# Kernel optimization log

Measured on AMD Instinct MI355X. Metric: run time of the kernel, lower is better.

Reference implementation:

```python
import jax, jax.numpy as jnp
import numpy as np

BINS = 8
EPS = 1e-12  # torch F.normalize default eps


def _pairwise_scores(matf):
    # torch: input1[a,b]=matf[b]; transpose(0,1)->matf[a]; transpose(-2,-1)->matf[a]^T [M,F]
    # matmul with input1[a,b]=matf[b] -> scores[a,b] = matf[a]^T @ matf[b], shape [M,M]
    bs, F, M = matf.shape
    s = jnp.einsum('afm,bfn->abmn', matf, matf)  # [bs, bs, M, M]
    return s.reshape(bs * bs, M * M)


def _histc_rows(x, bins):
    # torch.histc semantics with min=max=0: range = [row.min(), row.max()],
    # values == max land in the last bin.
    mn = jnp.min(x, axis=1, keepdims=True)
    mx = jnp.max(x, axis=1, keepdims=True)
    denom = jnp.where(mx > mn, mx - mn, jnp.ones_like(mx))
    idx = jnp.clip(jnp.floor((x - mn) / denom * bins).astype(jnp.int32), 0, bins - 1)
    nbs = x.shape[0]
    flat = (idx + (jnp.arange(nbs, dtype=jnp.int32) * bins)[:, None]).ravel()
    h = jnp.zeros(nbs * bins, dtype=x.dtype).at[flat].add(1.0)
    return h.reshape(nbs, bins)


def _l2_normalize(h):
    n = jnp.linalg.norm(h, axis=-1, keepdims=True)
    return h / jnp.maximum(n, EPS)


def setup_inputs() -> dict:
    key = jax.random.key(0)
    k1, k2 = jax.random.split(key)
    bs, F, M = 64, 256, 128
    matf1 = jax.random.normal(k1, (bs, F, M), dtype=jnp.float32)
    matf2 = jax.random.normal(k2, (bs, F, M), dtype=jnp.float32)
    return {"matf1": matf1, "matf2": matf2}


def reference(matf1, matf2):
    # scores are .detach()ed in the original; stop_gradient for faithfulness
    scores1 = jax.lax.stop_gradient(_pairwise_scores(matf1))  # [nbs, M*M]
    scores2 = jax.lax.stop_gradient(_pairwise_scores(matf2))
    h1 = _l2_normalize(_histc_rows(scores1, BINS))  # [nbs, 8]
    h2 = _l2_normalize(_histc_rows(scores2, BINS))
    return jnp.concatenate([h1, h2], axis=-1)  # [nbs, 16]
```

## Files before the change

kernel.cpp:

```cpp
#include <hip/hip_runtime.h>
#include <math.h>

#define BS 64
#define F  256
#define M  128
#define MF (M * F)
#define NBP 1056

typedef unsigned short u16;
typedef _Float16 f16x8 __attribute__((ext_vector_type(8)));
typedef float    f32x16 __attribute__((ext_vector_type(16)));

__global__ __launch_bounds__(256) void convert_f16_kernel(
    const float* __restrict__ m1, const float* __restrict__ m2,
    u16* __restrict__ hT)
{
    __shared__ float tile[64 * M];
    const int mat = blockIdx.x >> 6;
    const int b   = blockIdx.x & 63;
    const int f0  = blockIdx.y * 64;
    const float* src = (mat == 0 ? m1 : m2) + (size_t)b * MF + (size_t)f0 * M;
    const int tid = threadIdx.x;

    const float4* g = (const float4*)src;
    float4* s = (float4*)tile;
    #pragma unroll
    for (int i = 0; i < 8; ++i)
        s[tid + i * 256] = g[tid + i * 256];
    __syncthreads();

    const size_t obase = ((size_t)(mat * BS + b) * 32 + (f0 >> 3)) * 1024;
    #pragma unroll
    for (int it = 0; it < 4; ++it) {
        const int idx = it * 256 + tid;
        const int f8l = idx >> 7;
        const int m   = idx & 127;
        u16 hh[8] __attribute__((aligned(16)));
        #pragma unroll
        for (int j = 0; j < 8; ++j) {
            const float x = tile[(f8l * 8 + j) * M + m];
            const _Float16 h = (_Float16)x;
            hh[j] = __builtin_bit_cast(u16, h);
        }
        *(uint4*)&hT[obase + (size_t)idx * 8] = *(const uint4*)hh;
    }
}


#define KBAR() {                                              \
    asm volatile("s_waitcnt lgkmcnt(0)" ::: "memory");        \
    __builtin_amdgcn_s_barrier();                             \
    __builtin_amdgcn_sched_barrier(0);                        \
}

#define LOADB_S(SLOT, CH) {                                   \
    const u16* pbk = pb + (CH) * 4096;                        \
    bF[SLOT][0][0] = *(const f16x8*)(pbk);                    \
    bF[SLOT][0][1] = *(const f16x8*)(pbk + 256);              \
    bF[SLOT][1][0] = *(const f16x8*)(pbk + 2048);             \
    bF[SLOT][1][1] = *(const f16x8*)(pbk + 2048 + 256);       \
}

#define CHUNK(C) {                                                            \
    if ((C) <= 5) {                                                           \
        rA[(C) & 1][0] = *(const uint4*)(pa + ((C) + 2) * 4096);              \
        rA[(C) & 1][1] = *(const uint4*)(pa + ((C) + 2) * 4096 + 2048);       \
    }                                                                         \
    {                                                                         \
        const int cb = ((C) % 3) * 4096;                                      \
        _Pragma("unroll")                                                     \
        for (int kk = 0; kk < 2; ++kk) {                                      \
            const int base = cb + kk * 2048 + lhalf * 1024 + l31 * 8;         \
            f16x8 af[4];                                                      \
            _Pragma("unroll")                                                 \
            for (int t = 0; t < 4; ++t)                                       \
                af[t] = *(const f16x8*)&lds[base + t * 256];                  \
            _Pragma("unroll")                                                 \
            for (int ti = 0; ti < 4; ++ti) {                                  \
                acc[ti][0] = __builtin_amdgcn_mfma_f32_32x32x16_f16(af[ti], bF[(C) % 3][kk][0], acc[ti][0], 0, 0, 0); \
                acc[ti][1] = __builtin_amdgcn_mfma_f32_32x32x16_f16(af[ti], bF[(C) % 3][kk][1], acc[ti][1], 0, 0, 0); \
            }                                                                 \
        }                                                                     \
    }                                                                         \
    if ((C) <= 4) LOADB_S((C) % 3, (C) + 3);                                  \
    if ((C) <= 6) {                                                           \
        const int nb = (((C) + 1) % 3) * 4096;                                \
        *(uint4*)&lds[nb + d0] = rA[((C) + 1) & 1][0];                        \
        *(uint4*)&lds[nb + d1] = rA[((C) + 1) & 1][1];                        \
        KBAR();                                                               \
    }                                                                         \
}

__global__ __launch_bounds__(256, 2) void gram_hist_mfma(
    const u16* __restrict__ hT, float* __restrict__ out)
{
    __shared__ u16 lds[3 * 4096];
    __shared__ float smin[4], smax[4];
    __shared__ int hist[2][8];

    const int tid  = threadIdx.x;
    const int lane = tid & 63;
    const int w    = tid >> 6;

    if (tid < 16) hist[tid >> 3][tid & 7] = 0;

    const int bid  = blockIdx.x;
    const int xcd  = bid & 7;
    const int mat  = xcd >> 2;
    int p = (xcd & 3) * 264 + (bid >> 3);
    int a = 0;
    { int cnt = 32; while (p >= cnt) { p -= cnt; ++a; cnt = (64 - a + 1) >> 1; } }
    const int b1 = a + 2 * p;
    int b2 = b1 + 1;
    const bool b2valid = (b2 <= 63);
    if (!b2valid) b2 = b1;

    const int pp = w >> 1;
    const int c  = w & 1;
    const int l31   = lane & 31;
    const int lhalf = lane >> 5;

    const u16* pa = hT + (size_t)(mat * BS + a) * MF + tid * 8;
    const int d0 = tid * 8;
    const int d1 = (256 + tid) * 8;

    const int bsel = pp ? b2 : b1;
    const u16* pb = hT + (size_t)(mat * BS + bsel) * MF
                  + (size_t)(lhalf * 1024 + c * 512 + l31 * 8);

    f32x16 acc[4][2];
    #pragma unroll
    for (int ti = 0; ti < 4; ++ti)
        #pragma unroll
        for (int u = 0; u < 2; ++u)
            #pragma unroll
            for (int r = 0; r < 16; ++r) acc[ti][u][r] = 0.0f;

    uint4 rA[2][2];
    f16x8 bF[3][2][2];

    rA[0][0] = *(const uint4*)(pa);
    rA[0][1] = *(const uint4*)(pa + 2048);
    rA[1][0] = *(const uint4*)(pa + 4096);
    rA[1][1] = *(const uint4*)(pa + 4096 + 2048);
    LOADB_S(0, 0);
    LOADB_S(1, 1);
    LOADB_S(2, 2);
    *(uint4*)&lds[d0] = rA[0][0];
    *(uint4*)&lds[d1] = rA[0][1];
    KBAR();

    CHUNK(0); CHUNK(1); CHUNK(2); CHUNK(3);
    CHUNK(4); CHUNK(5); CHUNK(6); CHUNK(7);

    float vmin = acc[0][0][0], vmax = vmin;
    #pragma unroll
    for (int ti = 0; ti < 4; ++ti)
        #pragma unroll
        for (int u = 0; u < 2; ++u)
            #pragma unroll
            for (int r = 0; r < 16; ++r) {
                vmin = fminf(vmin, acc[ti][u][r]);
                vmax = fmaxf(vmax, acc[ti][u][r]);
            }
    #pragma unroll
    for (int off = 1; off < 64; off <<= 1) {
        vmin = fminf(vmin, __shfl_xor(vmin, off, 64));
        vmax = fmaxf(vmax, __shfl_xor(vmax, off, 64));
    }
    if (lane == 0) { smin[w] = vmin; smax[w] = vmax; }
    __syncthreads();
    const float pmn = fminf(smin[pp * 2], smin[pp * 2 + 1]);
    const float pmx = fmaxf(smax[pp * 2], smax[pp * 2 + 1]);
    const float denom = (pmx > pmn) ? (pmx - pmn) : 1.0f;
    const float scale = 8.0f / denom;
    const float bias  = -pmn * scale;

    unsigned w0 = 0, w1 = 0;
    #pragma unroll
    for (int ti = 0; ti < 4; ++ti)
        #pragma unroll
        for (int u = 0; u < 2; ++u)
            #pragma unroll
            for (int r = 0; r < 16; ++r) {
                const float t = fmaf(acc[ti][u][r], scale, bias);
                int k = (int)t;
                k = k > 7 ? 7 : k;
                const unsigned inc = 1u << ((k & 3) * 8);
                if (k < 4) w0 += inc; else w1 += inc;
            }
    unsigned e0 = (w0 & 0xFFu)         | (((w0 >> 8)  & 0xFFu) << 16);
    unsigned e1 = ((w0 >> 16) & 0xFFu) | (((w0 >> 24) & 0xFFu) << 16);
    unsigned e2 = (w1 & 0xFFu)         | (((w1 >> 8)  & 0xFFu) << 16);
    unsigned e3 = ((w1 >> 16) & 0xFFu) | (((w1 >> 24) & 0xFFu) << 16);
    #pragma unroll
    for (int off = 32; off > 0; off >>= 1) {
        e0 += __shfl_down(e0, off, 64);
        e1 += __shfl_down(e1, off, 64);
        e2 += __shfl_down(e2, off, 64);
        e3 += __shfl_down(e3, off, 64);
    }
    if (lane == 0) {
        atomicAdd(&hist[pp][0], (int)(e0 & 0xFFFFu)); atomicAdd(&hist[pp][1], (int)(e0 >> 16));
        atomicAdd(&hist[pp][2], (int)(e1 & 0xFFFFu)); atomicAdd(&hist[pp][3], (int)(e1 >> 16));
        atomicAdd(&hist[pp][4], (int)(e2 & 0xFFFFu)); atomicAdd(&hist[pp][5], (int)(e2 >> 16));
        atomicAdd(&hist[pp][6], (int)(e3 & 0xFFFFu)); atomicAdd(&hist[pp][7], (int)(e3 >> 16));
    }
    __syncthreads();

    const int B = (pp == 0) ? b1 : b2;
    const bool valid = (pp == 0) || b2valid;
    if (valid && c == 0 && lane < 8) {
        float ss = 0.0f;
        #pragma unroll
        for (int k = 0; k < 8; ++k) {
            const float cc = (float)hist[pp][k];
            ss += cc * cc;
        }
        const float nrm = fmaxf(sqrtf(ss), 1e-12f);
        const float v = (float)hist[pp][lane] / nrm;
        out[((size_t)a * BS + B) * 16 + mat * 8 + lane] = v;
        if (a != B)
            out[((size_t)B * BS + a) * 16 + mat * 8 + lane] = v;
    }
}

extern "C" void kernel_launch(void* const* d_in, const int* in_sizes, int n_in,
                              void* d_out, int out_size, void* d_ws, size_t ws_size,
                              hipStream_t stream) {
    const float* m1 = (const float*)d_in[0];
    const float* m2 = (const float*)d_in[1];
    float* out = (float*)d_out;

    u16* hT = (u16*)d_ws;

    convert_f16_kernel<<<dim3(128, 4), 256, 0, stream>>>(m1, m2, hT);
    gram_hist_mfma<<<2 * NBP, 256, 0, stream>>>(hT, out);
}
```

Measured before the change: 119.3 us.

## Stage A and B tiles into LDS via async global_load_lds with 512-thread blocks

Replaces the register-staged A loads and per-wave direct B fragment loads with async global-to-LDS loads (global_load_lds) for A, B1 and B2 into a triple-buffered LDS ring, synchronized by vmcnt waits and barriers. Blocks grow from 256 to 512 threads, with 8 waves each computing a 64x64 quadrant (2x2 MFMA tiles) instead of 4 waves doing 128x64. MFMA sections are wrapped in s_setprio. The intent is to cut VGPR use and register round-trips and to overlap memory with compute. The cost is larger LDS usage (72KB per block), which may limit occupancy.

Measured after the change: 124.1 us. 1.04x slower.

```diff
diff --git a/kernel.cpp b/kernel.cpp
--- a/kernel.cpp
+++ b/kernel.cpp
@@ -10,6 +10,9 @@
 typedef unsigned short u16;
 typedef _Float16 f16x8 __attribute__((ext_vector_type(8)));
 typedef float    f32x16 __attribute__((ext_vector_type(16)));
+
+typedef const __attribute__((address_space(1))) void gas_t;
+typedef __attribute__((address_space(3))) void las_t;
 
 __global__ __launch_bounds__(256) void convert_f16_kernel(
     const float* __restrict__ m1, const float* __restrict__ m2,
@@ -47,55 +50,46 @@
 }
 
 
-#define KBAR() {                                              \
-    asm volatile("s_waitcnt lgkmcnt(0)" ::: "memory");        \
-    __builtin_amdgcn_s_barrier();                             \
-    __builtin_amdgcn_sched_barrier(0);                        \
-}
-
-#define LOADB_S(SLOT, CH) {                                   \
-    const u16* pbk = pb + (CH) * 4096;                        \
-    bF[SLOT][0][0] = *(const f16x8*)(pbk);                    \
-    bF[SLOT][0][1] = *(const f16x8*)(pbk + 256);              \
-    bF[SLOT][1][0] = *(const f16x8*)(pbk + 2048);             \
-    bF[SLOT][1][1] = *(const f16x8*)(pbk + 2048 + 256);       \
-}
-
-#define CHUNK(C) {                                                            \
-    if ((C) <= 5) {                                                           \
-        rA[(C) & 1][0] = *(const uint4*)(pa + ((C) + 2) * 4096);              \
-        rA[(C) & 1][1] = *(const uint4*)(pa + ((C) + 2) * 4096 + 2048);       \
-    }                                                                         \
+#define ISSUE(S, TB) {                                                        \
+    __builtin_amdgcn_global_load_lds((gas_t*)(src0 + (S) * 4096),             \
+        (las_t*)&lds[(TB) + dst0], 16, 0, 0);                                 \
+    __builtin_amdgcn_global_load_lds((gas_t*)(src1 + (S) * 4096),             \
+        (las_t*)&lds[(TB) + dst1], 16, 0, 0);                                 \
+    __builtin_amdgcn_global_load_lds((gas_t*)(src2 + (S) * 4096),             \
+        (las_t*)&lds[(TB) + dst2], 16, 0, 0);                                 \
+}
+
+#define DOCHUNK(S) {                                                          \
+    if ((S) < 7) { asm volatile("s_waitcnt vmcnt(3)" ::: "memory"); }         \
+    else         { asm volatile("s_waitcnt vmcnt(0)" ::: "memory"); }         \
+    __builtin_amdgcn_s_barrier();                                             \
+    __builtin_amdgcn_sched_barrier(0);                                        \
     {                                                                         \
-        const int cb = ((C) % 3) * 4096;                                      \
+        const int bu = ((S) % 3) * 12288;                                     \
+        __builtin_amdgcn_s_setprio(1);                                        \
         _Pragma("unroll")                                                     \
         for (int kk = 0; kk < 2; ++kk) {                                      \
-            const int base = cb + kk * 2048 + lhalf * 1024 + l31 * 8;         \
-            f16x8 af[4];                                                      \
-            _Pragma("unroll")                                                 \
-            for (int t = 0; t < 4; ++t)                                       \
-                af[t] = *(const f16x8*)&lds[base + t * 256];                  \
-            _Pragma("unroll")                                                 \
-            for (int ti = 0; ti < 4; ++ti) {                                  \
-                acc[ti][0] = __builtin_amdgcn_mfma_f32_32x32x16_f16(af[ti], bF[(C) % 3][kk][0], acc[ti][0], 0, 0, 0); \
-                acc[ti][1] = __builtin_amdgcn_mfma_f32_32x32x16_f16(af[ti], bF[(C) % 3][kk][1], acc[ti][1], 0, 0, 0); \
-            }                                                                 \
+            const int kb = bu + kk * 2048 + lhalf * 1024;                     \
+            const f16x8 a0 = *(const f16x8*)&lds[kb + qr * 512 + l31 * 8];    \
+            const f16x8 a1 = *(const f16x8*)&lds[kb + qr * 512 + 256 + l31 * 8]; \
+            const f16x8 b0 = *(const f16x8*)&lds[kb + brow + qc * 512 + l31 * 8]; \
+            const f16x8 b1 = *(const f16x8*)&lds[kb + brow + qc * 512 + 256 + l31 * 8]; \
+            acc[0][0] = __builtin_amdgcn_mfma_f32_32x32x16_f16(a0, b0, acc[0][0], 0, 0, 0); \
+            acc[0][1] = __builtin_amdgcn_mfma_f32_32x32x16_f16(a0, b1, acc[0][1], 0, 0, 0); \
+            acc[1][0] = __builtin_amdgcn_mfma_f32_32x32x16_f16(a1, b0, acc[1][0], 0, 0, 0); \
+            acc[1][1] = __builtin_amdgcn_mfma_f32_32x32x16_f16(a1, b1, acc[1][1], 0, 0, 0); \
         }                                                                     \
+        __builtin_amdgcn_s_setprio(0);                                        \
     }                                                                         \
-    if ((C) <= 4) LOADB_S((C) % 3, (C) + 3);                                  \
-    if ((C) <= 6) {                                                           \
-        const int nb = (((C) + 1) % 3) * 4096;                                \
-        *(uint4*)&lds[nb + d0] = rA[((C) + 1) & 1][0];                        \
-        *(uint4*)&lds[nb + d1] = rA[((C) + 1) & 1][1];                        \
-        KBAR();                                                               \
-    }                                                                         \
-}
-
-__global__ __launch_bounds__(256, 2) void gram_hist_mfma(
+    __builtin_amdgcn_sched_barrier(0);                                        \
+    if ((S) <= 5) { ISSUE((S) + 2, (((S) + 2) % 3) * 12288); }                \
+}
+
+__global__ __launch_bounds__(512, 4) void gram_hist_mfma(
     const u16* __restrict__ hT, float* __restrict__ out)
 {
-    __shared__ u16 lds[3 * 4096];
-    __shared__ float smin[4], smax[4];
+    __shared__ u16 lds[3 * 12288];
+    __shared__ float smin[8], smax[8];
     __shared__ int hist[2][8];
 
     const int tid  = threadIdx.x;
@@ -115,53 +109,50 @@
     const bool b2valid = (b2 <= 63);
     if (!b2valid) b2 = b1;
 
-    const int pp = w >> 1;
-    const int c  = w & 1;
+    const int pp = w >> 2;
+    const int q  = w & 3;
+    const int qr = q >> 1;
+    const int qc = q & 1;
     const int l31   = lane & 31;
     const int lhalf = lane >> 5;
-
-    const u16* pa = hT + (size_t)(mat * BS + a) * MF + tid * 8;
-    const int d0 = tid * 8;
-    const int d1 = (256 + tid) * 8;
-
-    const int bsel = pp ? b2 : b1;
-    const u16* pb = hT + (size_t)(mat * BS + bsel) * MF
-                  + (size_t)(lhalf * 1024 + c * 512 + l31 * 8);
-
-    f32x16 acc[4][2];
-    #pragma unroll
-    for (int ti = 0; ti < 4; ++ti)
+    const int brow  = (1 + pp) * 4096;
+
+    const int g0 = w * 3, g1 = w * 3 + 1, g2 = w * 3 + 2;
+    const int r0_ = g0 >> 3, r1_ = g1 >> 3, r2_ = g2 >> 3;
+    const int s0_ = g0 & 7,  s1_ = g1 & 7,  s2_ = g2 & 7;
+    const int row0 = (r0_ == 0) ? a : (r0_ == 1 ? b1 : b2);
+    const int row1 = (r1_ == 0) ? a : (r1_ == 1 ? b1 : b2);
+    const int row2 = (r2_ == 0) ? a : (r2_ == 1 ? b1 : b2);
+    const u16* src0 = hT + (size_t)(mat * BS + row0) * MF + s0_ * 512 + lane * 8;
+    const u16* src1 = hT + (size_t)(mat * BS + row1) * MF + s1_ * 512 + lane * 8;
+    const u16* src2 = hT + (size_t)(mat * BS + row2) * MF + s2_ * 512 + lane * 8;
+    const int dst0 = r0_ * 4096 + s0_ * 512;
+    const int dst1 = r1_ * 4096 + s1_ * 512;
+    const int dst2 = r2_ * 4096 + s2_ * 512;
+
+    f32x16 acc[2][2];
+    #pragma unroll
+    for (int t = 0; t < 2; ++t)
         #pragma unroll
         for (int u = 0; u < 2; ++u)
             #pragma unroll
-            for (int r = 0; r < 16; ++r) acc[ti][u][r] = 0.0f;
-
-    uint4 rA[2][2];
-    f16x8 bF[3][2][2];
-
-    rA[0][0] = *(const uint4*)(pa);
-    rA[0][1] = *(const uint4*)(pa + 2048);
-    rA[1][0] = *(const uint4*)(pa + 4096);
-    rA[1][1] = *(const uint4*)(pa + 4096 + 2048);
-    LOADB_S(0, 0);
-    LOADB_S(1, 1);
-    LOADB_S(2, 2);
-    *(uint4*)&lds[d0] = rA[0][0];
-    *(uint4*)&lds[d1] = rA[0][1];
-    KBAR();
-
-    CHUNK(0); CHUNK(1); CHUNK(2); CHUNK(3);
-    CHUNK(4); CHUNK(5); CHUNK(6); CHUNK(7);
+            for (int r = 0; r < 16; ++r) acc[t][u][r] = 0.0f;
+
+    ISSUE(0, 0);
+    ISSUE(1, 12288);
+
+    DOCHUNK(0); DOCHUNK(1); DOCHUNK(2); DOCHUNK(3);
+    DOCHUNK(4); DOCHUNK(5); DOCHUNK(6); DOCHUNK(7);
 
     float vmin = acc[0][0][0], vmax = vmin;
     #pragma unroll
-    for (int ti = 0; ti < 4; ++ti)
+    for (int t = 0; t < 2; ++t)
         #pragma unroll
         for (int u = 0; u < 2; ++u)
             #pragma unroll
             for (int r = 0; r < 16; ++r) {
-                vmin = fminf(vmin, acc[ti][u][r]);
-                vmax = fmaxf(vmax, acc[ti][u][r]);
+                vmin = fminf(vmin, acc[t][u][r]);
+                vmax = fmaxf(vmax, acc[t][u][r]);
             }
     #pragma unroll
     for (int off = 1; off < 64; off <<= 1) {
@@ -170,21 +161,24 @@
     }
     if (lane == 0) { smin[w] = vmin; smax[w] = vmax; }
     __syncthreads();
-    const float pmn = fminf(smin[pp * 2], smin[pp * 2 + 1]);
-    const float pmx = fmaxf(smax[pp * 2], smax[pp * 2 + 1]);
+    const int p4 = pp * 4;
+    const float pmn = fminf(fminf(smin[p4], smin[p4 + 1]),
+                            fminf(smin[p4 + 2], smin[p4 + 3]));
+    const float pmx = fmaxf(fmaxf(smax[p4], smax[p4 + 1]),
+                            fmaxf(smax[p4 + 2], smax[p4 + 3]));
     const float denom = (pmx > pmn) ? (pmx - pmn) : 1.0f;
     const float scale = 8.0f / denom;
     const float bias  = -pmn * scale;
 
     unsigned w0 = 0, w1 = 0;
     #pragma unroll
-    for (int ti = 0; ti < 4; ++ti)
+    for (int t = 0; t < 2; ++t)
         #pragma unroll
         for (int u = 0; u < 2; ++u)
             #pragma unroll
             for (int r = 0; r < 16; ++r) {
-                const float t = fmaf(acc[ti][u][r], scale, bias);
-                int k = (int)t;
+                const float tv = fmaf(acc[t][u][r], scale, bias);
+                int k = (int)tv;
                 k = k > 7 ? 7 : k;
                 const unsigned inc = 1u << ((k & 3) * 8);
                 if (k < 4) w0 += inc; else w1 += inc;
@@ -210,7 +204,7 @@
 
     const int B = (pp == 0) ? b1 : b2;
     const bool valid = (pp == 0) || b2valid;
-    if (valid && c == 0 && lane < 8) {
+    if (valid && q == 0 && lane < 8) {
         float ss = 0.0f;
         #pragma unroll
         for (int k = 0; k < 8; ++k) {
@@ -235,5 +229,5 @@
     u16* hT = (u16*)d_ws;
 
     convert_f16_kernel<<<dim3(128, 4), 256, 0, stream>>>(m1, m2, hT);
-    gram_hist_mfma<<<2 * NBP, 256, 0, stream>>>(hT, out);
-}
+    gram_hist_mfma<<<2 * NBP, 512, 0, stream>>>(hT, out);
+}
```

## Stream A and B tiles into LDS with direct global-to-LDS async loads

Applied to the files above, without the earlier changes.

Replaces the register-staged A tile and the per-wave B register prefetch with global_load_lds DMA transfers of the A, B1 and B2 chunks into a triple-buffered LDS ring, kept two chunks ahead using vmcnt waits. B fragments are now read from LDS rather than held in registers, and the MFMA section runs at raised wave priority via s_setprio. The aim is to cut VGPR pressure and the ds_write plus wait overhead, and to overlap loading with compute. In exchange, LDS use grows threefold, which may limit occupancy at two blocks per CU, and B now takes extra LDS reads.

Measured after the change: 120.7 us. Within noise of the previous version (+1.2%).

```diff
diff --git a/kernel.cpp b/kernel.cpp
--- a/kernel.cpp
+++ b/kernel.cpp
@@ -10,6 +10,9 @@
 typedef unsigned short u16;
 typedef _Float16 f16x8 __attribute__((ext_vector_type(8)));
 typedef float    f32x16 __attribute__((ext_vector_type(16)));
+
+typedef const __attribute__((address_space(1))) void gas_t;
+typedef __attribute__((address_space(3))) void las_t;
 
 __global__ __launch_bounds__(256) void convert_f16_kernel(
     const float* __restrict__ m1, const float* __restrict__ m2,
@@ -47,54 +50,54 @@
 }
 
 
-#define KBAR() {                                              \
-    asm volatile("s_waitcnt lgkmcnt(0)" ::: "memory");        \
-    __builtin_amdgcn_s_barrier();                             \
-    __builtin_amdgcn_sched_barrier(0);                        \
-}
-
-#define LOADB_S(SLOT, CH) {                                   \
-    const u16* pbk = pb + (CH) * 4096;                        \
-    bF[SLOT][0][0] = *(const f16x8*)(pbk);                    \
-    bF[SLOT][0][1] = *(const f16x8*)(pbk + 256);              \
-    bF[SLOT][1][0] = *(const f16x8*)(pbk + 2048);             \
-    bF[SLOT][1][1] = *(const f16x8*)(pbk + 2048 + 256);       \
-}
-
-#define CHUNK(C) {                                                            \
-    if ((C) <= 5) {                                                           \
-        rA[(C) & 1][0] = *(const uint4*)(pa + ((C) + 2) * 4096);              \
-        rA[(C) & 1][1] = *(const uint4*)(pa + ((C) + 2) * 4096 + 2048);       \
-    }                                                                         \
+#define ISSUE(S, RB) {                                                        \
+    __builtin_amdgcn_global_load_lds((gas_t*)(sp0 + (S) * 4096),              \
+        (las_t*)&lds[(RB) + dq0], 16, 0, 0);                                  \
+    __builtin_amdgcn_global_load_lds((gas_t*)(sp1 + (S) * 4096),              \
+        (las_t*)&lds[(RB) + dq1], 16, 0, 0);                                  \
+    __builtin_amdgcn_global_load_lds((gas_t*)(sp2 + (S) * 4096),              \
+        (las_t*)&lds[(RB) + dq2], 16, 0, 0);                                  \
+    __builtin_amdgcn_global_load_lds((gas_t*)(sp3 + (S) * 4096),              \
+        (las_t*)&lds[(RB) + dq3], 16, 0, 0);                                  \
+    __builtin_amdgcn_global_load_lds((gas_t*)(sp4 + (S) * 4096),              \
+        (las_t*)&lds[(RB) + dq4], 16, 0, 0);                                  \
+    __builtin_amdgcn_global_load_lds((gas_t*)(sp5 + (S) * 4096),              \
+        (las_t*)&lds[(RB) + dq5], 16, 0, 0);                                  \
+}
+
+#define DOCHUNK(S) {                                                          \
+    if ((S) < 7) { asm volatile("s_waitcnt vmcnt(6)" ::: "memory"); }         \
+    else         { asm volatile("s_waitcnt vmcnt(0)" ::: "memory"); }         \
+    __builtin_amdgcn_s_barrier();                                             \
+    __builtin_amdgcn_sched_barrier(0);                                        \
     {                                                                         \
-        const int cb = ((C) % 3) * 4096;                                      \
+        const int rb = ((S) % 3) * 12288;                                     \
+        __builtin_amdgcn_s_setprio(1);                                        \
         _Pragma("unroll")                                                     \
         for (int kk = 0; kk < 2; ++kk) {                                      \
-            const int base = cb + kk * 2048 + lhalf * 1024 + l31 * 8;         \
-            f16x8 af[4];                                                      \
+            const int ab = rb + kk * 2048 + lhalf * 1024 + l31 * 8;           \
+            const int bb = rb + brow + kk * 2048 + lhalf * 1024 + c * 512 + l31 * 8; \
+            f16x8 af[4], bf[2];                                               \
             _Pragma("unroll")                                                 \
             for (int t = 0; t < 4; ++t)                                       \
-                af[t] = *(const f16x8*)&lds[base + t * 256];                  \
+                af[t] = *(const f16x8*)&lds[ab + t * 256];                    \
+            bf[0] = *(const f16x8*)&lds[bb];                                  \
+            bf[1] = *(const f16x8*)&lds[bb + 256];                            \
             _Pragma("unroll")                                                 \
             for (int ti = 0; ti < 4; ++ti) {                                  \
-                acc[ti][0] = __builtin_amdgcn_mfma_f32_32x32x16_f16(af[ti], bF[(C) % 3][kk][0], acc[ti][0], 0, 0, 0); \
-                acc[ti][1] = __builtin_amdgcn_mfma_f32_32x32x16_f16(af[ti], bF[(C) % 3][kk][1], acc[ti][1], 0, 0, 0); \
+                acc[ti][0] = __builtin_amdgcn_mfma_f32_32x32x16_f16(af[ti], bf[0], acc[ti][0], 0, 0, 0); \
+                acc[ti][1] = __builtin_amdgcn_mfma_f32_32x32x16_f16(af[ti], bf[1], acc[ti][1], 0, 0, 0); \
             }                                                                 \
         }                                                                     \
+        __builtin_amdgcn_s_setprio(0);                                        \
     }                                                                         \
-    if ((C) <= 4) LOADB_S((C) % 3, (C) + 3);                                  \
-    if ((C) <= 6) {                                                           \
-        const int nb = (((C) + 1) % 3) * 4096;                                \
-        *(uint4*)&lds[nb + d0] = rA[((C) + 1) & 1][0];                        \
-        *(uint4*)&lds[nb + d1] = rA[((C) + 1) & 1][1];                        \
-        KBAR();                                                               \
-    }                                                                         \
+    if ((S) <= 5) { ISSUE((S) + 2, (((S) + 2) % 3) * 12288); }                \
 }
 
 __global__ __launch_bounds__(256, 2) void gram_hist_mfma(
     const u16* __restrict__ hT, float* __restrict__ out)
 {
-    __shared__ u16 lds[3 * 4096];
+    __shared__ u16 lds[3 * 12288];
     __shared__ float smin[4], smax[4];
     __shared__ int hist[2][8];
 
@@ -119,14 +122,25 @@
     const int c  = w & 1;
     const int l31   = lane & 31;
     const int lhalf = lane >> 5;
-
-    const u16* pa = hT + (size_t)(mat * BS + a) * MF + tid * 8;
-    const int d0 = tid * 8;
-    const int d1 = (256 + tid) * 8;
-
-    const int bsel = pp ? b2 : b1;
-    const u16* pb = hT + (size_t)(mat * BS + bsel) * MF
-                  + (size_t)(lhalf * 1024 + c * 512 + l31 * 8);
+    const int brow  = (1 + pp) * 4096;
+
+    const u16* rowp[3];
+    rowp[0] = hT + (size_t)(mat * BS + a)  * MF;
+    rowp[1] = hT + (size_t)(mat * BS + b1) * MF;
+    rowp[2] = hT + (size_t)(mat * BS + b2) * MF;
+    const int g0 = w * 6;
+    const u16* sp0 = rowp[(g0 + 0) >> 3] + ((g0 + 0) & 7) * 512 + lane * 8;
+    const u16* sp1 = rowp[(g0 + 1) >> 3] + ((g0 + 1) & 7) * 512 + lane * 8;
+    const u16* sp2 = rowp[(g0 + 2) >> 3] + ((g0 + 2) & 7) * 512 + lane * 8;
+    const u16* sp3 = rowp[(g0 + 3) >> 3] + ((g0 + 3) & 7) * 512 + lane * 8;
+    const u16* sp4 = rowp[(g0 + 4) >> 3] + ((g0 + 4) & 7) * 512 + lane * 8;
+    const u16* sp5 = rowp[(g0 + 5) >> 3] + ((g0 + 5) & 7) * 512 + lane * 8;
+    const int dq0 = ((g0 + 0) >> 3) * 4096 + ((g0 + 0) & 7) * 512;
+    const int dq1 = ((g0 + 1) >> 3) * 4096 + ((g0 + 1) & 7) * 512;
+    const int dq2 = ((g0 + 2) >> 3) * 4096 + ((g0 + 2) & 7) * 512;
+    const int dq3 = ((g0 + 3) >> 3) * 4096 + ((g0 + 3) & 7) * 512;
+    const int dq4 = ((g0 + 4) >> 3) * 4096 + ((g0 + 4) & 7) * 512;
+    const int dq5 = ((g0 + 5) >> 3) * 4096 + ((g0 + 5) & 7) * 512;
 
     f32x16 acc[4][2];
     #pragma unroll
@@ -136,22 +150,11 @@
             #pragma unroll
             for (int r = 0; r < 16; ++r) acc[ti][u][r] = 0.0f;
 
-    uint4 rA[2][2];
-    f16x8 bF[3][2][2];
-
-    rA[0][0] = *(const uint4*)(pa);
-    rA[0][1] = *(const uint4*)(pa + 2048);
-    rA[1][0] = *(const uint4*)(pa + 4096);
-    rA[1][1] = *(const uint4*)(pa + 4096 + 2048);
-    LOADB_S(0, 0);
-    LOADB_S(1, 1);
-    LOADB_S(2, 2);
-    *(uint4*)&lds[d0] = rA[0][0];
-    *(uint4*)&lds[d1] = rA[0][1];
-    KBAR();
-
-    CHUNK(0); CHUNK(1); CHUNK(2); CHUNK(3);
-    CHUNK(4); CHUNK(5); CHUNK(6); CHUNK(7);
+    ISSUE(0, 0);
+    ISSUE(1, 12288);
+
+    DOCHUNK(0); DOCHUNK(1); DOCHUNK(2); DOCHUNK(3);
+    DOCHUNK(4); DOCHUNK(5); DOCHUNK(6); DOCHUNK(7);
 
     float vmin = acc[0][0][0], vmax = vmin;
     #pragma unroll
```
